# Kernel optimization log

Measured on AMD Instinct MI355X. Metric: run time of the kernel, lower is better.

Reference implementation:

```python
import jax, jax.numpy as jnp
import numpy as np

IMG = 448
GRID = 32          # num_grids = image_size // patch_size
HID = 1024         # mm_hidden_size
B = 64
# (expert_input_image_size, expert_patch, expert_hidden)
EXPERTS = [(448, 14, 1024), (336, 14, 768), (448, 32, 1152)]


def resize_ac(x, oh, ow):
    """Bilinear resize with align_corners=True on last two dims. x: [..., H, W]."""
    h, w = x.shape[-2], x.shape[-1]
    if (h, w) == (oh, ow):
        return x
    ys = jnp.linspace(0.0, h - 1.0, oh)
    xs = jnp.linspace(0.0, w - 1.0, ow)
    y0 = jnp.floor(ys).astype(jnp.int32); y1 = jnp.clip(y0 + 1, 0, h - 1)
    x0 = jnp.floor(xs).astype(jnp.int32); x1 = jnp.clip(x0 + 1, 0, w - 1)
    ty = (ys - y0).astype(x.dtype); tx = (xs - x0).astype(x.dtype)
    rows = x[..., y0, :] * (1 - ty)[:, None] + x[..., y1, :] * ty[:, None]  # [..., oh, W]
    return rows[..., x0] * (1 - tx) + rows[..., x1] * tx                     # [..., oh, ow]


def _forward(x, selected_experts, routing_weights, towers):
    b = x.shape[0]
    out = jnp.zeros((b, GRID * GRID * HID), x.dtype)
    for i, (s, p, c) in enumerate(EXPERTS):
        wt, bt, wp, bp = towers[i]
        xi = resize_ac(x, s, s)  # resize input if expert image size differs (identity otherwise)
        g = s // p
        # patch-embed vision tower: [b,3,s,s] -> [b, g*g, 3*p*p] -> [b, g*g, c]
        patches = xi.reshape(b, 3, g, p, g, p).transpose(0, 2, 4, 1, 3, 5).reshape(b, g * g, 3 * p * p)
        feat = patches @ wt + bt
        # 3D -> [b, c, g, g], resize feature grid to shared num_grids
        feat = feat.transpose(0, 2, 1).reshape(b, c, g, g)
        feat = resize_ac(feat, GRID, GRID)
        # projector over tokens: [b, T, c] @ [c, HID]
        feat = feat.reshape(b, c, GRID * GRID).transpose(0, 2, 1) @ wp + bp
        feat = feat.reshape(b, -1)
        # dense-masked combine (== torch.where gather/scatter with disjoint top-k experts)
        w_i = jnp.sum(jnp.where(selected_experts == i, routing_weights,
                                jnp.zeros((), routing_weights.dtype)), axis=1)
        out = out + w_i[:, None] * feat
    return out.reshape(b, GRID * GRID, HID)


def setup_inputs() -> dict:
    key = jax.random.key(0)
    ks = jax.random.split(key, 20)
    inp = {}
    inp["x"] = jax.random.normal(ks[0], (B, 3, IMG, IMG), jnp.float32)
    # top-2 of 3 experts per sample, distinct within a row (matches scatter semantics)
    e0 = jax.random.randint(ks[1], (B, 1), 0, 3)
    e1 = (e0 + 1 + jax.random.randint(ks[2], (B, 1), 0, 2)) % 3
    inp["selected_experts"] = jnp.concatenate([e0, e1], axis=1)
    rw = jax.random.uniform(ks[3], (B, 2), jnp.float32)
    inp["routing_weights"] = rw / rw.sum(axis=1, keepdims=True)
    for i, (s, p, c) in enumerate(EXPERTS):
        inp[f"w_tower_{i}"] = 0.02 * jax.random.normal(ks[4 + 4 * i], (3 * p * p, c), jnp.float32)
        inp[f"b_tower_{i}"] = jnp.zeros((c,), jnp.float32)
        inp[f"w_proj_{i}"] = 0.02 * jax.random.normal(ks[5 + 4 * i], (c, HID), jnp.float32)
        inp[f"b_proj_{i}"] = jnp.zeros((HID,), jnp.float32)
    return inp


def reference(x, selected_experts, routing_weights,
              w_tower_0, b_tower_0, w_proj_0, b_proj_0,
              w_tower_1, b_tower_1, w_proj_1, b_proj_1,
              w_tower_2, b_tower_2, w_proj_2, b_proj_2):
    towers = [(w_tower_0, b_tower_0, w_proj_0, b_proj_0),
              (w_tower_1, b_tower_1, w_proj_1, b_proj_1),
              (w_tower_2, b_tower_2, w_proj_2, b_proj_2)]
    return _forward(x, selected_experts, routing_weights, towers)
```

## Files before the change

kernel.cpp:

```cpp
#include <hip/hip_runtime.h>
#include <cstddef>
#include <cstdint>


#define HID 1024

typedef __bf16 bf16x8 __attribute__((ext_vector_type(8)));
typedef float f32x4 __attribute__((ext_vector_type(4)));

__device__ __forceinline__ unsigned short f2bf(float f) {
  union { float f; unsigned u; } v; v.f = f;
  unsigned r = v.u + 0x7fffu + ((v.u >> 16) & 1u);
  return (unsigned short)(r >> 16);
}
__device__ __forceinline__ float bf2f(unsigned h) {
  union { unsigned u; float f; } v; v.u = h << 16;
  return v.f;
}
__device__ __forceinline__ void gld16(const unsigned short* g, unsigned short* l) {
  auto gp = (const __attribute__((address_space(1))) unsigned int*)(const void*)g;
  auto lp = (__attribute__((address_space(3))) unsigned int*)(void*)l;
  __builtin_amdgcn_global_load_lds(gp, lp, 16, 0, 0);
}

__device__ __forceinline__ int2 swz128() {
  int gx = gridDim.x;
  int nwg = gx * gridDim.y;
  int lin = (int)(blockIdx.y * gx + blockIdx.x);
  int q = nwg >> 3, r = nwg & 7;
  int xcd = lin & 7, idx = lin >> 3;
  int wg = (xcd < r ? xcd * (q + 1) : r * (q + 1) + (xcd - r) * q) + idx;
  return make_int2((wg % gx) * 128, (wg / gx) * 128);
}

__global__ void k_weights(const int* __restrict__ sel, const float* __restrict__ rw,
                          float* __restrict__ w3) {
  int b = threadIdx.x;
  if (b < 64) {
    float w0 = 0.f, w1 = 0.f, w2 = 0.f;
    for (int k = 0; k < 2; ++k) {
      int e = sel[b * 2 + k];
      float r = rw[b * 2 + k];
      if (e == 0) w0 += r; else if (e == 1) w1 += r; else w2 += r;
    }
    w3[b * 3 + 0] = w0; w3[b * 3 + 1] = w1; w3[b * 3 + 2] = w2;
  }
}

__global__ void k_cbias(const float* __restrict__ w3, const float* __restrict__ b0,
                        const float* __restrict__ b1, const float* __restrict__ b2,
                        float* __restrict__ cb) {
  int s = blockIdx.x;
  float w0 = w3[s * 3], w1 = w3[s * 3 + 1], w2 = w3[s * 3 + 2];
  for (int n = threadIdx.x; n < HID; n += 256)
    cb[s * HID + n] = w0 * b0[n] + w1 * b1[n] + w2 * b2[n];
}

__global__ void k_tables(int* __restrict__ koff, int* __restrict__ rowoff,
                         int4* __restrict__ stok, float4* __restrict__ wco,
                         int S, int P, int G, int T, int bch, int K, int Kp) {
  int idx = blockIdx.x * 256 + threadIdx.x;
  if (idx < Kp) {
    if (idx < K) {
      int pp = P * P;
      int ch = idx / pp;
      int r = idx - ch * pp;
      int py = r / P;
      int px = r - py * P;
      koff[idx] = ch * S * S + py * S + px;
    } else koff[idx] = 0;
  }
  int nro = bch * T;
  if (idx < nro) {
    int bl = idx / T;
    int t = idx - bl * T;
    int gy = t / G;
    int gx = t - gy * G;
    rowoff[idx] = bl * 3 * S * S + gy * P * S + gx * P;
  }
  if (idx < 1024) {
    int oy = idx >> 5, ox = idx & 31;
    float sc = (float)(G - 1) / 31.0f;
    float fy = oy * sc, fx = ox * sc;
    int y0 = (int)floorf(fy), x0 = (int)floorf(fx);
    float ty = fy - y0, tx = fx - x0;
    int y1 = min(y0 + 1, G - 1), x1 = min(x0 + 1, G - 1);
    stok[idx] = make_int4(y0 * G + x0, y0 * G + x1, y1 * G + x0, y1 * G + x1);
    wco[idx] = make_float4((1.f - ty) * (1.f - tx), (1.f - ty) * tx,
                           ty * (1.f - tx), ty * tx);
  }
}

__global__ void k_resize_img(const float* __restrict__ x, unsigned short* __restrict__ o,
                             int total) {
  int idx = blockIdx.x * 256 + threadIdx.x;
  if (idx >= total) return;
  int ox = idx % 336;
  int t = idx / 336;
  int oy = t % 336;
  int bc = t / 336;
  const float sc = 447.0f / 335.0f;
  float fy = oy * sc, fx = ox * sc;
  int y0 = (int)floorf(fy), x0 = (int)floorf(fx);
  float ty = fy - y0, tx = fx - x0;
  int y1 = min(y0 + 1, 447), x1 = min(x0 + 1, 447);
  const float* p = x + (size_t)bc * 448 * 448;
  float v00 = p[y0 * 448 + x0], v01 = p[y0 * 448 + x1];
  float v10 = p[y1 * 448 + x0], v11 = p[y1 * 448 + x1];
  float r0 = v00 * (1.f - ty) + v10 * ty;
  float r1 = v01 * (1.f - ty) + v11 * ty;
  o[idx] = f2bf(r0 * (1.f - tx) + r1 * tx);
}

__global__ void k_pack_w(const float* __restrict__ W, unsigned short* __restrict__ Wp,
                         int K, int N, int Kp) {
  __shared__ float t[32][33];
  int kb = blockIdx.x * 32, nb = blockIdx.y * 32;
  int tx = threadIdx.x & 31, ty = threadIdx.x >> 5;
#pragma unroll
  for (int r = 0; r < 32; r += 8) {
    int k = kb + ty + r, n = nb + tx;
    t[ty + r][tx] = (k < K) ? W[(size_t)k * N + n] : 0.f;
  }
  __syncthreads();
#pragma unroll
  for (int r = 0; r < 32; r += 8) {
    int n = nb + ty + r, k = kb + tx;
    if (k < Kp) Wp[(size_t)n * Kp + k] = f2bf(t[tx][ty + r]);
  }
}

__global__ void k_im2col_f32(const float* __restrict__ img, unsigned short* __restrict__ Ap,
                             const int* __restrict__ rowoff, const int* __restrict__ koff,
                             int M, int K, int Kp) {
  int k2 = (blockIdx.y * 256 + threadIdx.x) * 2;
  if (k2 >= Kp) return;
  int m = blockIdx.x;
  unsigned v = 0;
  if (m < M && k2 < K) {
    float2 f = *(const float2*)(const void*)&img[rowoff[m] + koff[k2]];
    v = (unsigned)f2bf(f.x) | ((unsigned)f2bf(f.y) << 16);
  }
  *(unsigned*)(void*)&Ap[(size_t)m * Kp + k2] = v;
}

__global__ void k_im2col_bf16(const unsigned short* __restrict__ img,
                              unsigned short* __restrict__ Ap,
                              const int* __restrict__ rowoff, const int* __restrict__ koff,
                              int M, int K, int Kp) {
  int k2 = (blockIdx.y * 256 + threadIdx.x) * 2;
  if (k2 >= Kp) return;
  int m = blockIdx.x;
  unsigned v = 0;
  if (m < M && k2 < K)
    v = *(const unsigned*)(const void*)&img[rowoff[m] + koff[k2]];
  *(unsigned*)(void*)&Ap[(size_t)m * Kp + k2] = v;
}

__global__ __launch_bounds__(256) void k_tower(
    const unsigned short* __restrict__ Ap, const unsigned short* __restrict__ Wp,
    const float* __restrict__ bias, unsigned short* __restrict__ Fp,
    int N, int Kp) {
  __shared__ __align__(16) unsigned short As[128 * 32];
  __shared__ __align__(16) unsigned short Bs[128 * 32];
  int tid = threadIdx.x, wave = tid >> 6, lane = tid & 63;
  int2 sw = swz128();
  int n0 = sw.x, m0 = sw.y;

  const unsigned short* arow0 = Ap + (size_t)(m0 + (tid >> 2)) * Kp + (tid & 3) * 8;
  const unsigned short* arow1 = arow0 + (size_t)64 * Kp;
  const unsigned short* wrow0 = Wp + (size_t)(n0 + (tid >> 2)) * Kp + (tid & 3) * 8;
  const unsigned short* wrow1 = wrow0 + (size_t)64 * Kp;
  unsigned short* AsW0 = As + wave * 512;
  unsigned short* AsW1 = As + 2048 + wave * 512;
  unsigned short* BsW0 = Bs + wave * 512;
  unsigned short* BsW1 = Bs + 2048 + wave * 512;

  int wm = (wave >> 1) << 6, wn = (wave & 1) << 6;
  int fm = lane & 15, fq = (lane >> 4) << 3;
  f32x4 acc[4][4] = {};

  for (int kb = 0; kb < Kp; kb += 32) {
    __syncthreads();
    gld16(arow0 + kb, AsW0);
    gld16(arow1 + kb, AsW1);
    gld16(wrow0 + kb, BsW0);
    gld16(wrow1 + kb, BsW1);
    __syncthreads();
    bf16x8 af[4], bfr[4];
#pragma unroll
    for (int i = 0; i < 4; ++i) af[i] = *(const bf16x8*)&As[(wm + i * 16 + fm) * 32 + fq];
#pragma unroll
    for (int j = 0; j < 4; ++j) bfr[j] = *(const bf16x8*)&Bs[(wn + j * 16 + fm) * 32 + fq];
#pragma unroll
    for (int i = 0; i < 4; ++i)
#pragma unroll
      for (int j = 0; j < 4; ++j)
        acc[i][j] = __builtin_amdgcn_mfma_f32_16x16x32_bf16(af[i], bfr[j], acc[i][j], 0, 0, 0);
  }

  int mq = (lane >> 4) << 2;
#pragma unroll
  for (int i = 0; i < 4; ++i) {
    int mbase = m0 + wm + i * 16 + mq;
#pragma unroll
    for (int j = 0; j < 4; ++j) {
      int n = n0 + wn + j * 16 + fm;
      float bsv = bias[n];
      f32x4 v = acc[i][j];
#pragma unroll
      for (int r = 0; r < 4; ++r)
        Fp[(size_t)(mbase + r) * N + n] = f2bf(v[r] + bsv);
    }
  }
}

__global__ void k_feat_resize(const unsigned short* __restrict__ C1,
                              unsigned short* __restrict__ F,
                              const int4* __restrict__ stok, const float4* __restrict__ wco,
                              int Tsrc, int C) {
  int bt = blockIdx.x;
  int bl = bt >> 10, t = bt & 1023;
  int4 s = stok[t];
  float4 w = wco[t];
  const unsigned* b32 = (const unsigned*)(C1 + (size_t)bl * Tsrc * C);
  unsigned* o32 = (unsigned*)(F + (size_t)bt * C);
  int C2 = C >> 1;
  int r0 = s.x * C2, r1 = s.y * C2, r2 = s.z * C2, r3 = s.w * C2;
  for (int c = threadIdx.x; c < C2; c += 256) {
    unsigned p0 = b32[r0 + c], p1 = b32[r1 + c], p2 = b32[r2 + c], p3 = b32[r3 + c];
    float lo = w.x * bf2f(p0 & 0xffffu) + w.y * bf2f(p1 & 0xffffu) +
               w.z * bf2f(p2 & 0xffffu) + w.w * bf2f(p3 & 0xffffu);
    float hi = w.x * bf2f(p0 >> 16) + w.y * bf2f(p1 >> 16) +
               w.z * bf2f(p2 >> 16) + w.w * bf2f(p3 >> 16);
    o32[c] = (unsigned)f2bf(lo) | ((unsigned)f2bf(hi) << 16);
  }
}

__global__ __launch_bounds__(256) void k_proj3(
    const unsigned short* __restrict__ A0, const unsigned short* __restrict__ A1,
    const unsigned short* __restrict__ A2,
    const unsigned short* __restrict__ W0, const unsigned short* __restrict__ W1,
    const unsigned short* __restrict__ W2,
    const float* __restrict__ cb, float* __restrict__ out,
    const float* __restrict__ w3, int b0) {
  __shared__ __align__(16) unsigned short As[128 * 32];
  __shared__ __align__(16) unsigned short Bs[128 * 32];
  int tid = threadIdx.x, wave = tid >> 6, lane = tid & 63;
  int2 sw = swz128();
  int n0 = sw.x, m0 = sw.y;
  int s = b0 + (m0 >> 10);
  float wg0 = w3[s * 3], wg1 = w3[s * 3 + 1], wg2 = w3[s * 3 + 2];
  const float wgs[3] = {wg0, wg1, wg2};
  const unsigned short* Ae[3] = {A0, A1, A2};
  const unsigned short* We[3] = {W0, W1, W2};
  const int Ke[3] = {1024, 768, 1152};

  unsigned short* AsW0 = As + wave * 512;
  unsigned short* AsW1 = As + 2048 + wave * 512;
  unsigned short* BsW0 = Bs + wave * 512;
  unsigned short* BsW1 = Bs + 2048 + wave * 512;
  int wm = (wave >> 1) << 6, wn = (wave & 1) << 6;
  int fm = lane & 15, fq = (lane >> 4) << 3;

  f32x4 accT[4][4] = {};

#pragma unroll
  for (int e = 0; e < 3; ++e) {
    float w = wgs[e];
    if (w == 0.f) continue;
    int K = Ke[e];
    const unsigned short* arow0 = Ae[e] + (size_t)(m0 + (tid >> 2)) * K + (tid & 3) * 8;
    const unsigned short* arow1 = arow0 + (size_t)64 * K;
    const unsigned short* wrow0 = We[e] + (size_t)(n0 + (tid >> 2)) * K + (tid & 3) * 8;
    const unsigned short* wrow1 = wrow0 + (size_t)64 * K;
    f32x4 acc[4][4] = {};
    for (int kb = 0; kb < K; kb += 32) {
      __syncthreads();
      gld16(arow0 + kb, AsW0);
      gld16(arow1 + kb, AsW1);
      gld16(wrow0 + kb, BsW0);
      gld16(wrow1 + kb, BsW1);
      __syncthreads();
      bf16x8 af[4], bfr[4];
#pragma unroll
      for (int i = 0; i < 4; ++i) af[i] = *(const bf16x8*)&As[(wm + i * 16 + fm) * 32 + fq];
#pragma unroll
      for (int j = 0; j < 4; ++j) bfr[j] = *(const bf16x8*)&Bs[(wn + j * 16 + fm) * 32 + fq];
#pragma unroll
      for (int i = 0; i < 4; ++i)
#pragma unroll
        for (int j = 0; j < 4; ++j)
          acc[i][j] = __builtin_amdgcn_mfma_f32_16x16x32_bf16(af[i], bfr[j], acc[i][j], 0, 0, 0);
    }
#pragma unroll
    for (int i = 0; i < 4; ++i)
#pragma unroll
      for (int j = 0; j < 4; ++j)
        accT[i][j] += w * acc[i][j];
  }

  int mq = (lane >> 4) << 2;
  float* obase = out + ((size_t)b0 * 1024 + (size_t)m0) * HID + n0;
  const float* cbs = cb + (size_t)s * HID + n0;
#pragma unroll
  for (int i = 0; i < 4; ++i) {
#pragma unroll
    for (int j = 0; j < 4; ++j) {
      int n = wn + j * 16 + fm;
      float cbv = cbs[n];
      f32x4 v = accT[i][j];
#pragma unroll
      for (int r = 0; r < 4; ++r)
        obase[(size_t)(wm + i * 16 + mq + r) * HID + n] = v[r] + cbv;
    }
  }
}

extern "C" void kernel_launch(void* const* d_in, const int* in_sizes, int n_in,
                              void* d_out, int out_size, void* d_ws, size_t ws_size,
                              hipStream_t stream) {
  (void)in_sizes; (void)n_in; (void)out_size;
  const float* x = (const float*)d_in[0];
  const int* sel = (const int*)d_in[1];
  const float* rw = (const float*)d_in[2];
  const float* wt[3] = {(const float*)d_in[3], (const float*)d_in[7], (const float*)d_in[11]};
  const float* bt[3] = {(const float*)d_in[4], (const float*)d_in[8], (const float*)d_in[12]};
  const float* wp[3] = {(const float*)d_in[5], (const float*)d_in[9], (const float*)d_in[13]};
  const float* bp[3] = {(const float*)d_in[6], (const float*)d_in[10], (const float*)d_in[14]};
  float* out = (float*)d_out;

  char* ws = (char*)d_ws;
  size_t off = 0;
  auto alloc = [&](size_t bytes) -> void* {
    off = (off + 255) & ~(size_t)255;
    void* p = ws + off;
    off += bytes;
    return p;
  };
  auto ceil128 = [](size_t m) -> size_t { return (m + 127) & ~(size_t)127; };

  float* w3 = (float*)alloc(64 * 3 * 4);
  float* cb = (float*)alloc((size_t)64 * HID * 4);
  int* koff0 = (int*)alloc(608 * 4);
  int* koff1 = (int*)alloc(608 * 4);
  int* koff2 = (int*)alloc(3072 * 4);
  int* ro0 = (int*)alloc((size_t)64 * 1024 * 4);
  int* ro1 = (int*)alloc((size_t)64 * 576 * 4);
  int* ro2 = (int*)alloc((size_t)64 * 196 * 4);
  int4* st1 = (int4*)alloc(1024 * 16);
  float4* wc1 = (float4*)alloc(1024 * 16);
  int4* st2 = (int4*)alloc(1024 * 16);
  float4* wc2 = (float4*)alloc(1024 * 16);
  unsigned short* wt0p = (unsigned short*)alloc((size_t)1024 * 608 * 2);
  unsigned short* wt1p = (unsigned short*)alloc((size_t)768 * 608 * 2);
  unsigned short* wt2p = (unsigned short*)alloc((size_t)1152 * 3072 * 2);
  unsigned short* wp0p = (unsigned short*)alloc((size_t)1024 * 1024 * 2);
  unsigned short* wp1p = (unsigned short*)alloc((size_t)1024 * 768 * 2);
  unsigned short* wp2p = (unsigned short*)alloc((size_t)1024 * 1152 * 2);
  size_t fixed_end = off;

  auto scratch_elems = [&](int bc) -> size_t {
    size_t a0 = (size_t)bc * 1024 * 608;
    size_t a1 = (size_t)bc * 3 * 336 * 336 + ceil128((size_t)bc * 576) * 608;
    size_t a2 = ceil128((size_t)bc * 196) * (3072 + 1152);
    size_t m = a0 > a1 ? a0 : a1;
    return m > a2 ? m : a2;
  };
  auto need = [&](int bc) -> size_t {
    size_t el = (size_t)bc * 1024 * (1024 + 768 + 1152) + scratch_elems(bc);
    return el * 2 + 16 * 512;
  };
  int bch = 64;
  while (bch > 1 && fixed_end + need(bch) > ws_size) bch >>= 1;
  unsigned short* F0 = (unsigned short*)alloc((size_t)bch * 1024 * 1024 * 2);
  unsigned short* F1 = (unsigned short*)alloc((size_t)bch * 1024 * 768 * 2);
  unsigned short* F2 = (unsigned short*)alloc((size_t)bch * 1024 * 1152 * 2);
  unsigned short* scratch = (unsigned short*)alloc(scratch_elems(bch) * 2);

  int M1 = bch * 576, Mp1 = (int)ceil128((size_t)M1);
  int M2 = bch * 196, Mp2 = (int)ceil128((size_t)M2);
  unsigned short* x336 = scratch;
  unsigned short* Apad1 = scratch + (size_t)bch * 3 * 336 * 336;
  unsigned short* Apad2 = scratch;
  unsigned short* Ftow2 = scratch + (size_t)Mp2 * 3072;
  unsigned short* Ftow1 = F2;

  k_weights<<<1, 64, 0, stream>>>(sel, rw, w3);
  k_cbias<<<64, 256, 0, stream>>>(w3, bp[0], bp[1], bp[2], cb);
  {
    int n0 = max(608, max(bch * 1024, 1024));
    int n1 = max(608, max(bch * 576, 1024));
    int n2 = max(3072, max(bch * 196, 1024));
    k_tables<<<(n0 + 255) / 256, 256, 0, stream>>>(koff0, ro0, st1, wc1, 448, 14, 32, 1024, bch, 588, 608);
    k_tables<<<(n1 + 255) / 256, 256, 0, stream>>>(koff1, ro1, st1, wc1, 336, 14, 24, 576, bch, 588, 608);
    k_tables<<<(n2 + 255) / 256, 256, 0, stream>>>(koff2, ro2, st2, wc2, 448, 32, 14, 196, bch, 3072, 3072);
  }
  k_pack_w<<<dim3(608 / 32, 1024 / 32), 256, 0, stream>>>(wt[0], wt0p, 588, 1024, 608);
  k_pack_w<<<dim3(608 / 32, 768 / 32), 256, 0, stream>>>(wt[1], wt1p, 588, 768, 608);
  k_pack_w<<<dim3(3072 / 32, 1152 / 32), 256, 0, stream>>>(wt[2], wt2p, 3072, 1152, 3072);
  k_pack_w<<<dim3(1024 / 32, 1024 / 32), 256, 0, stream>>>(wp[0], wp0p, 1024, 1024, 1024);
  k_pack_w<<<dim3(768 / 32, 1024 / 32), 256, 0, stream>>>(wp[1], wp1p, 768, 1024, 768);
  k_pack_w<<<dim3(1152 / 32, 1024 / 32), 256, 0, stream>>>(wp[2], wp2p, 1152, 1024, 1152);

  int nchunk = 64 / bch;
  for (int c = 0; c < nchunk; ++c) {
    int b0 = c * bch;
    const float* xc = x + (size_t)b0 * 3 * 448 * 448;

    {
      int M = bch * 1024;
      k_im2col_f32<<<dim3(M, 2), 256, 0, stream>>>(xc, scratch, ro0, koff0, M, 588, 608);
      k_tower<<<dim3(1024 / 128, M / 128), 256, 0, stream>>>(scratch, wt0p, bt[0], F0, 1024, 608);
    }
    {
      int tot = bch * 3 * 336 * 336;
      k_resize_img<<<(tot + 255) / 256, 256, 0, stream>>>(xc, x336, tot);
      k_im2col_bf16<<<dim3(Mp1, 2), 256, 0, stream>>>(x336, Apad1, ro1, koff1, M1, 588, 608);
      k_tower<<<dim3(768 / 128, Mp1 / 128), 256, 0, stream>>>(Apad1, wt1p, bt[1], Ftow1, 768, 608);
      k_feat_resize<<<bch * 1024, 256, 0, stream>>>(Ftow1, F1, st1, wc1, 576, 768);
    }
    {
      k_im2col_f32<<<dim3(Mp2, 6), 256, 0, stream>>>(xc, Apad2, ro2, koff2, M2, 3072, 3072);
      k_tower<<<dim3(1152 / 128, Mp2 / 128), 256, 0, stream>>>(Apad2, wt2p, bt[2], Ftow2, 1152, 3072);
      k_feat_resize<<<bch * 1024, 256, 0, stream>>>(Ftow2, F2, st2, wc2, 196, 1152);
    }
    k_proj3<<<dim3(HID / 128, bch * 1024 / 128), 256, 0, stream>>>(
        F0, F1, F2, wp0p, wp1p, wp2p, cb, out, w3, b0);
  }
}
```

Baseline: 1.551 ms.

## Project before resizing for experts 1/2 and skip work for unrouted samples

Bilinear feature-grid resize is linear and commutes with the token projection. So experts 1 and 2 now run the projection GEMM on their native 576/196 tokens instead of 1024 resized tokens, and the resize and weighted combine happen on fp32 outputs in a new combine kernel. Image resize, im2col, tower and projection kernels now return early for samples whose routing weight for that expert is zero, which removes unrouted work. This adds an fp32 intermediate buffer and extra read-modify-write traffic on the output. The order of rounding and bias application also changes slightly.

```diff
diff --git a/kernel.cpp b/kernel.cpp
--- a/kernel.cpp
+++ b/kernel.cpp
@@ -92,13 +92,13 @@
 }
 
 __global__ void k_resize_img(const float* __restrict__ x, unsigned short* __restrict__ o,
-                             int total) {
+                             int total, const float* __restrict__ w3, int b0) {
   int idx = blockIdx.x * 256 + threadIdx.x;
   if (idx >= total) return;
+  int bc = idx / (336 * 336);
+  if (w3[(b0 + bc / 3) * 3 + 1] == 0.f) return;
   int ox = idx % 336;
-  int t = idx / 336;
-  int oy = t % 336;
-  int bc = t / 336;
+  int oy = (idx / 336) % 336;
   const float sc = 447.0f / 335.0f;
   float fy = oy * sc, fx = ox * sc;
   int y0 = (int)floorf(fy), x0 = (int)floorf(fx);
@@ -132,12 +132,15 @@
 
 __global__ void k_im2col_f32(const float* __restrict__ img, unsigned short* __restrict__ Ap,
                              const int* __restrict__ rowoff, const int* __restrict__ koff,
-                             int M, int K, int Kp) {
+                             int M, int K, int Kp,
+                             const float* __restrict__ w3, int b0, int e, int T) {
+  int m = blockIdx.x;
+  if (m >= M) return;
+  if (w3[(b0 + m / T) * 3 + e] == 0.f) return;
   int k2 = (blockIdx.y * 256 + threadIdx.x) * 2;
   if (k2 >= Kp) return;
-  int m = blockIdx.x;
   unsigned v = 0;
-  if (m < M && k2 < K) {
+  if (k2 < K) {
     float2 f = *(const float2*)(const void*)&img[rowoff[m] + koff[k2]];
     v = (unsigned)f2bf(f.x) | ((unsigned)f2bf(f.y) << 16);
   }
@@ -147,12 +150,15 @@
 __global__ void k_im2col_bf16(const unsigned short* __restrict__ img,
                               unsigned short* __restrict__ Ap,
                               const int* __restrict__ rowoff, const int* __restrict__ koff,
-                              int M, int K, int Kp) {
+                              int M, int K, int Kp,
+                              const float* __restrict__ w3, int b0, int e, int T) {
+  int m = blockIdx.x;
+  if (m >= M) return;
+  if (w3[(b0 + m / T) * 3 + e] == 0.f) return;
   int k2 = (blockIdx.y * 256 + threadIdx.x) * 2;
   if (k2 >= Kp) return;
-  int m = blockIdx.x;
   unsigned v = 0;
-  if (m < M && k2 < K)
+  if (k2 < K)
     v = *(const unsigned*)(const void*)&img[rowoff[m] + koff[k2]];
   *(unsigned*)(void*)&Ap[(size_t)m * Kp + k2] = v;
 }
@@ -160,12 +166,20 @@
 __global__ __launch_bounds__(256) void k_tower(
     const unsigned short* __restrict__ Ap, const unsigned short* __restrict__ Wp,
     const float* __restrict__ bias, unsigned short* __restrict__ Fp,
-    int N, int Kp) {
+    int N, int Kp, const float* __restrict__ w3, int b0, int e, int T, int bch) {
   __shared__ __align__(16) unsigned short As[128 * 32];
   __shared__ __align__(16) unsigned short Bs[128 * 32];
   int tid = threadIdx.x, wave = tid >> 6, lane = tid & 63;
   int2 sw = swz128();
   int n0 = sw.x, m0 = sw.y;
+
+  {
+    int s0 = m0 / T, s1 = (m0 + 127) / T;
+    if (s1 >= bch) s1 = bch - 1;
+    bool act = false;
+    for (int s = s0; s <= s1; ++s) act |= (w3[(b0 + s) * 3 + e] != 0.f);
+    if (!act) return;
+  }
 
   const unsigned short* arow0 = Ap + (size_t)(m0 + (tid >> 2)) * Kp + (tid & 3) * 8;
   const unsigned short* arow1 = arow0 + (size_t)64 * Kp;
@@ -215,33 +229,8 @@
   }
 }
 
-__global__ void k_feat_resize(const unsigned short* __restrict__ C1,
-                              unsigned short* __restrict__ F,
-                              const int4* __restrict__ stok, const float4* __restrict__ wco,
-                              int Tsrc, int C) {
-  int bt = blockIdx.x;
-  int bl = bt >> 10, t = bt & 1023;
-  int4 s = stok[t];
-  float4 w = wco[t];
-  const unsigned* b32 = (const unsigned*)(C1 + (size_t)bl * Tsrc * C);
-  unsigned* o32 = (unsigned*)(F + (size_t)bt * C);
-  int C2 = C >> 1;
-  int r0 = s.x * C2, r1 = s.y * C2, r2 = s.z * C2, r3 = s.w * C2;
-  for (int c = threadIdx.x; c < C2; c += 256) {
-    unsigned p0 = b32[r0 + c], p1 = b32[r1 + c], p2 = b32[r2 + c], p3 = b32[r3 + c];
-    float lo = w.x * bf2f(p0 & 0xffffu) + w.y * bf2f(p1 & 0xffffu) +
-               w.z * bf2f(p2 & 0xffffu) + w.w * bf2f(p3 & 0xffffu);
-    float hi = w.x * bf2f(p0 >> 16) + w.y * bf2f(p1 >> 16) +
-               w.z * bf2f(p2 >> 16) + w.w * bf2f(p3 >> 16);
-    o32[c] = (unsigned)f2bf(lo) | ((unsigned)f2bf(hi) << 16);
-  }
-}
-
-__global__ __launch_bounds__(256) void k_proj3(
-    const unsigned short* __restrict__ A0, const unsigned short* __restrict__ A1,
-    const unsigned short* __restrict__ A2,
-    const unsigned short* __restrict__ W0, const unsigned short* __restrict__ W1,
-    const unsigned short* __restrict__ W2,
+__global__ __launch_bounds__(256) void k_proj0(
+    const unsigned short* __restrict__ A, const unsigned short* __restrict__ W,
     const float* __restrict__ cb, float* __restrict__ out,
     const float* __restrict__ w3, int b0) {
   __shared__ __align__(16) unsigned short As[128 * 32];
@@ -250,71 +239,159 @@
   int2 sw = swz128();
   int n0 = sw.x, m0 = sw.y;
   int s = b0 + (m0 >> 10);
-  float wg0 = w3[s * 3], wg1 = w3[s * 3 + 1], wg2 = w3[s * 3 + 2];
-  const float wgs[3] = {wg0, wg1, wg2};
-  const unsigned short* Ae[3] = {A0, A1, A2};
-  const unsigned short* We[3] = {W0, W1, W2};
-  const int Ke[3] = {1024, 768, 1152};
-
+  float w0 = w3[s * 3];
+  float* obase = out + ((size_t)b0 * 1024 + (size_t)m0) * HID + n0;
+  const float* cbs = cb + (size_t)s * HID + n0;
+  if (w0 == 0.f) {
+    for (int idx = tid; idx < 128 * 32; idx += 256) {
+      int rr = idx >> 5, cc = (idx & 31) << 2;
+      *(float4*)&obase[(size_t)rr * HID + cc] = *(const float4*)&cbs[cc];
+    }
+    return;
+  }
+  const int K = 1024;
+  const unsigned short* arow0 = A + (size_t)(m0 + (tid >> 2)) * K + (tid & 3) * 8;
+  const unsigned short* arow1 = arow0 + (size_t)64 * K;
+  const unsigned short* wrow0 = W + (size_t)(n0 + (tid >> 2)) * K + (tid & 3) * 8;
+  const unsigned short* wrow1 = wrow0 + (size_t)64 * K;
   unsigned short* AsW0 = As + wave * 512;
   unsigned short* AsW1 = As + 2048 + wave * 512;
   unsigned short* BsW0 = Bs + wave * 512;
   unsigned short* BsW1 = Bs + 2048 + wave * 512;
   int wm = (wave >> 1) << 6, wn = (wave & 1) << 6;
   int fm = lane & 15, fq = (lane >> 4) << 3;
-
-  f32x4 accT[4][4] = {};
-
-#pragma unroll
-  for (int e = 0; e < 3; ++e) {
-    float w = wgs[e];
-    if (w == 0.f) continue;
-    int K = Ke[e];
-    const unsigned short* arow0 = Ae[e] + (size_t)(m0 + (tid >> 2)) * K + (tid & 3) * 8;
-    const unsigned short* arow1 = arow0 + (size_t)64 * K;
-    const unsigned short* wrow0 = We[e] + (size_t)(n0 + (tid >> 2)) * K + (tid & 3) * 8;
-    const unsigned short* wrow1 = wrow0 + (size_t)64 * K;
-    f32x4 acc[4][4] = {};
-    for (int kb = 0; kb < K; kb += 32) {
-      __syncthreads();
-      gld16(arow0 + kb, AsW0);
-      gld16(arow1 + kb, AsW1);
-      gld16(wrow0 + kb, BsW0);
-      gld16(wrow1 + kb, BsW1);
-      __syncthreads();
-      bf16x8 af[4], bfr[4];
-#pragma unroll
-      for (int i = 0; i < 4; ++i) af[i] = *(const bf16x8*)&As[(wm + i * 16 + fm) * 32 + fq];
-#pragma unroll
-      for (int j = 0; j < 4; ++j) bfr[j] = *(const bf16x8*)&Bs[(wn + j * 16 + fm) * 32 + fq];
-#pragma unroll
-      for (int i = 0; i < 4; ++i)
-#pragma unroll
-        for (int j = 0; j < 4; ++j)
-          acc[i][j] = __builtin_amdgcn_mfma_f32_16x16x32_bf16(af[i], bfr[j], acc[i][j], 0, 0, 0);
-    }
+  f32x4 acc[4][4] = {};
+  for (int kb = 0; kb < K; kb += 32) {
+    __syncthreads();
+    gld16(arow0 + kb, AsW0);
+    gld16(arow1 + kb, AsW1);
+    gld16(wrow0 + kb, BsW0);
+    gld16(wrow1 + kb, BsW1);
+    __syncthreads();
+    bf16x8 af[4], bfr[4];
+#pragma unroll
+    for (int i = 0; i < 4; ++i) af[i] = *(const bf16x8*)&As[(wm + i * 16 + fm) * 32 + fq];
+#pragma unroll
+    for (int j = 0; j < 4; ++j) bfr[j] = *(const bf16x8*)&Bs[(wn + j * 16 + fm) * 32 + fq];
 #pragma unroll
     for (int i = 0; i < 4; ++i)
 #pragma unroll
       for (int j = 0; j < 4; ++j)
-        accT[i][j] += w * acc[i][j];
-  }
-
+        acc[i][j] = __builtin_amdgcn_mfma_f32_16x16x32_bf16(af[i], bfr[j], acc[i][j], 0, 0, 0);
+  }
   int mq = (lane >> 4) << 2;
-  float* obase = out + ((size_t)b0 * 1024 + (size_t)m0) * HID + n0;
-  const float* cbs = cb + (size_t)s * HID + n0;
 #pragma unroll
   for (int i = 0; i < 4; ++i) {
 #pragma unroll
     for (int j = 0; j < 4; ++j) {
       int n = wn + j * 16 + fm;
       float cbv = cbs[n];
-      f32x4 v = accT[i][j];
+      f32x4 v = acc[i][j];
 #pragma unroll
       for (int r = 0; r < 4; ++r)
-        obase[(size_t)(wm + i * 16 + mq + r) * HID + n] = v[r] + cbv;
-    }
-  }
+        obase[(size_t)(wm + i * 16 + mq + r) * HID + n] = w0 * v[r] + cbv;
+    }
+  }
+}
+
+__global__ __launch_bounds__(256) void k_projP(
+    const unsigned short* __restrict__ A, const unsigned short* __restrict__ W,
+    float* __restrict__ P, const float* __restrict__ w3,
+    int b0, int e, int T, int bch, int K) {
+  __shared__ __align__(16) unsigned short As[128 * 32];
+  __shared__ __align__(16) unsigned short Bs[128 * 32];
+  int tid = threadIdx.x, wave = tid >> 6, lane = tid & 63;
+  int2 sw = swz128();
+  int n0 = sw.x, m0 = sw.y;
+  {
+    int s0 = m0 / T, s1 = (m0 + 127) / T;
+    if (s1 >= bch) s1 = bch - 1;
+    bool act = false;
+    for (int s = s0; s <= s1; ++s) act |= (w3[(b0 + s) * 3 + e] != 0.f);
+    if (!act) return;
+  }
+  const unsigned short* arow0 = A + (size_t)(m0 + (tid >> 2)) * K + (tid & 3) * 8;
+  const unsigned short* arow1 = arow0 + (size_t)64 * K;
+  const unsigned short* wrow0 = W + (size_t)(n0 + (tid >> 2)) * K + (tid & 3) * 8;
+  const unsigned short* wrow1 = wrow0 + (size_t)64 * K;
+  unsigned short* AsW0 = As + wave * 512;
+  unsigned short* AsW1 = As + 2048 + wave * 512;
+  unsigned short* BsW0 = Bs + wave * 512;
+  unsigned short* BsW1 = Bs + 2048 + wave * 512;
+  int wm = (wave >> 1) << 6, wn = (wave & 1) << 6;
+  int fm = lane & 15, fq = (lane >> 4) << 3;
+  f32x4 acc[4][4] = {};
+  for (int kb = 0; kb < K; kb += 32) {
+    __syncthreads();
+    gld16(arow0 + kb, AsW0);
+    gld16(arow1 + kb, AsW1);
+    gld16(wrow0 + kb, BsW0);
+    gld16(wrow1 + kb, BsW1);
+    __syncthreads();
+    bf16x8 af[4], bfr[4];
+#pragma unroll
+    for (int i = 0; i < 4; ++i) af[i] = *(const bf16x8*)&As[(wm + i * 16 + fm) * 32 + fq];
+#pragma unroll
+    for (int j = 0; j < 4; ++j) bfr[j] = *(const bf16x8*)&Bs[(wn + j * 16 + fm) * 32 + fq];
+#pragma unroll
+    for (int i = 0; i < 4; ++i)
+#pragma unroll
+      for (int j = 0; j < 4; ++j)
+        acc[i][j] = __builtin_amdgcn_mfma_f32_16x16x32_bf16(af[i], bfr[j], acc[i][j], 0, 0, 0);
+  }
+  int mq = (lane >> 4) << 2;
+#pragma unroll
+  for (int i = 0; i < 4; ++i) {
+#pragma unroll
+    for (int j = 0; j < 4; ++j) {
+      int n = n0 + wn + j * 16 + fm;
+      f32x4 v = acc[i][j];
+#pragma unroll
+      for (int r = 0; r < 4; ++r)
+        P[(size_t)(m0 + wm + i * 16 + mq + r) * HID + n] = v[r];
+    }
+  }
+}
+
+__global__ void k_combine(float* __restrict__ out,
+                          const float* __restrict__ P1, const float* __restrict__ P2,
+                          const int4* __restrict__ st1, const float4* __restrict__ wc1,
+                          const int4* __restrict__ st2, const float4* __restrict__ wc2,
+                          const float* __restrict__ w3, int b0) {
+  int nwg = gridDim.x;
+  int lin = blockIdx.x;
+  int q = nwg >> 3;
+  int bt = (lin & 7) * q + (lin >> 3);
+  int s = bt >> 10, t = bt & 1023;
+  float w1 = w3[(b0 + s) * 3 + 1], w2 = w3[(b0 + s) * 3 + 2];
+  int n = threadIdx.x << 2;
+  float* op = out + ((size_t)(b0 + s) * 1024 + t) * HID + n;
+  float4 acc = *(float4*)op;
+  if (w1 != 0.f) {
+    int4 si = st1[t]; float4 wc = wc1[t];
+    const float* base = P1 + (size_t)s * 576 * HID + n;
+    float4 a = *(const float4*)&base[(size_t)si.x * HID];
+    float4 b = *(const float4*)&base[(size_t)si.y * HID];
+    float4 c = *(const float4*)&base[(size_t)si.z * HID];
+    float4 d = *(const float4*)&base[(size_t)si.w * HID];
+    acc.x += w1 * (wc.x * a.x + wc.y * b.x + wc.z * c.x + wc.w * d.x);
+    acc.y += w1 * (wc.x * a.y + wc.y * b.y + wc.z * c.y + wc.w * d.y);
+    acc.z += w1 * (wc.x * a.z + wc.y * b.z + wc.z * c.z + wc.w * d.z);
+    acc.w += w1 * (wc.x * a.w + wc.y * b.w + wc.z * c.w + wc.w * d.w);
+  }
+  if (w2 != 0.f) {
+    int4 si = st2[t]; float4 wc = wc2[t];
+    const float* base = P2 + (size_t)s * 196 * HID + n;
+    float4 a = *(const float4*)&base[(size_t)si.x * HID];
+    float4 b = *(const float4*)&base[(size_t)si.y * HID];
+    float4 c = *(const float4*)&base[(size_t)si.z * HID];
+    float4 d = *(const float4*)&base[(size_t)si.w * HID];
+    acc.x += w2 * (wc.x * a.x + wc.y * b.x + wc.z * c.x + wc.w * d.x);
+    acc.y += w2 * (wc.x * a.y + wc.y * b.y + wc.z * c.y + wc.w * d.y);
+    acc.z += w2 * (wc.x * a.z + wc.y * b.z + wc.z * c.z + wc.w * d.z);
+    acc.w += w2 * (wc.x * a.w + wc.y * b.w + wc.z * c.w + wc.w * d.w);
+  }
+  *(float4*)op = acc;
 }
 
 extern "C" void kernel_launch(void* const* d_in, const int* in_sizes, int n_in,
@@ -361,30 +438,32 @@
   size_t fixed_end = off;
 
   auto scratch_elems = [&](int bc) -> size_t {
-    size_t a0 = (size_t)bc * 1024 * 608;
-    size_t a1 = (size_t)bc * 3 * 336 * 336 + ceil128((size_t)bc * 576) * 608;
-    size_t a2 = ceil128((size_t)bc * 196) * (3072 + 1152);
-    size_t m = a0 > a1 ? a0 : a1;
-    return m > a2 ? m : a2;
+    size_t mp1 = ceil128((size_t)bc * 576), mp2 = ceil128((size_t)bc * 196);
+    size_t p0 = (size_t)bc * 1024 * 1024 + (size_t)bc * 1024 * 608;
+    size_t p1 = (size_t)bc * 338688 + mp1 * 608 + mp1 * 768;
+    size_t p2 = mp2 * 3072 + mp2 * 1152;
+    size_t m = p0 > p1 ? p0 : p1;
+    return m > p2 ? m : p2;
   };
   auto need = [&](int bc) -> size_t {
-    size_t el = (size_t)bc * 1024 * (1024 + 768 + 1152) + scratch_elems(bc);
-    return el * 2 + 16 * 512;
+    size_t mp1 = ceil128((size_t)bc * 576), mp2 = ceil128((size_t)bc * 196);
+    return scratch_elems(bc) * 2 + (mp1 + mp2) * (size_t)HID * 4 + 32 * 512;
   };
   int bch = 64;
   while (bch > 1 && fixed_end + need(bch) > ws_size) bch >>= 1;
-  unsigned short* F0 = (unsigned short*)alloc((size_t)bch * 1024 * 1024 * 2);
-  unsigned short* F1 = (unsigned short*)alloc((size_t)bch * 1024 * 768 * 2);
-  unsigned short* F2 = (unsigned short*)alloc((size_t)bch * 1024 * 1152 * 2);
+
+  size_t Mp1 = ceil128((size_t)bch * 576), Mp2 = ceil128((size_t)bch * 196);
   unsigned short* scratch = (unsigned short*)alloc(scratch_elems(bch) * 2);
-
-  int M1 = bch * 576, Mp1 = (int)ceil128((size_t)M1);
-  int M2 = bch * 196, Mp2 = (int)ceil128((size_t)M2);
+  float* P1 = (float*)alloc(Mp1 * HID * 4);
+  float* P2 = (float*)alloc(Mp2 * HID * 4);
+
+  unsigned short* Ftow0 = scratch;
+  unsigned short* Apad0 = scratch + (size_t)bch * 1024 * 1024;
   unsigned short* x336 = scratch;
-  unsigned short* Apad1 = scratch + (size_t)bch * 3 * 336 * 336;
+  unsigned short* Apad1 = scratch + (size_t)bch * 338688;
+  unsigned short* Ftow1 = Apad1 + Mp1 * 608;
   unsigned short* Apad2 = scratch;
-  unsigned short* Ftow2 = scratch + (size_t)Mp2 * 3072;
-  unsigned short* Ftow1 = F2;
+  unsigned short* Ftow2 = scratch + Mp2 * 3072;
 
   k_weights<<<1, 64, 0, stream>>>(sel, rw, w3);
   k_cbias<<<64, 256, 0, stream>>>(w3, bp[0], bp[1], bp[2], cb);
@@ -410,22 +489,32 @@
 
     {
       int M = bch * 1024;
-      k_im2col_f32<<<dim3(M, 2), 256, 0, stream>>>(xc, scratch, ro0, koff0, M, 588, 608);
-      k_tower<<<dim3(1024 / 128, M / 128), 256, 0, stream>>>(scratch, wt0p, bt[0], F0, 1024, 608);
+      k_im2col_f32<<<dim3(M, 2), 256, 0, stream>>>(xc, Apad0, ro0, koff0, M, 588, 608,
+                                                   w3, b0, 0, 1024);
+      k_tower<<<dim3(1024 / 128, M / 128), 256, 0, stream>>>(Apad0, wt0p, bt[0], Ftow0,
+                                                             1024, 608, w3, b0, 0, 1024, bch);
+      k_proj0<<<dim3(HID / 128, M / 128), 256, 0, stream>>>(Ftow0, wp0p, cb, out, w3, b0);
     }
     {
       int tot = bch * 3 * 336 * 336;
-      k_resize_img<<<(tot + 255) / 256, 256, 0, stream>>>(xc, x336, tot);
-      k_im2col_bf16<<<dim3(Mp1, 2), 256, 0, stream>>>(x336, Apad1, ro1, koff1, M1, 588, 608);
-      k_tower<<<dim3(768 / 128, Mp1 / 128), 256, 0, stream>>>(Apad1, wt1p, bt[1], Ftow1, 768, 608);
-      k_feat_resize<<<bch * 1024, 256, 0, stream>>>(Ftow1, F1, st1, wc1, 576, 768);
+      int M = bch * 576;
+      k_resize_img<<<(tot + 255) / 256, 256, 0, stream>>>(xc, x336, tot, w3, b0);
+      k_im2col_bf16<<<dim3(M, 2), 256, 0, stream>>>(x336, Apad1, ro1, koff1, M, 588, 608,
+                                                    w3, b0, 1, 576);
+      k_tower<<<dim3(768 / 128, (int)(Mp1 / 128)), 256, 0, stream>>>(
+          Apad1, wt1p, bt[1], Ftow1, 768, 608, w3, b0, 1, 576, bch);
+      k_projP<<<dim3(HID / 128, (int)(Mp1 / 128)), 256, 0, stream>>>(
+          Ftow1, wp1p, P1, w3, b0, 1, 576, bch, 768);
     }
     {
-      k_im2col_f32<<<dim3(Mp2, 6), 256, 0, stream>>>(xc, Apad2, ro2, koff2, M2, 3072, 3072);
-      k_tower<<<dim3(1152 / 128, Mp2 / 128), 256, 0, stream>>>(Apad2, wt2p, bt[2], Ftow2, 1152, 3072);
-      k_feat_resize<<<bch * 1024, 256, 0, stream>>>(Ftow2, F2, st2, wc2, 196, 1152);
-    }
-    k_proj3<<<dim3(HID / 128, bch * 1024 / 128), 256, 0, stream>>>(
-        F0, F1, F2, wp0p, wp1p, wp2p, cb, out, w3, b0);
-  }
-}
+      int M = bch * 196;
+      k_im2col_f32<<<dim3(M, 6), 256, 0, stream>>>(xc, Apad2, ro2, koff2, M, 3072, 3072,
+                                                   w3, b0, 2, 196);
+      k_tower<<<dim3(1152 / 128, (int)(Mp2 / 128)), 256, 0, stream>>>(
+          Apad2, wt2p, bt[2], Ftow2, 1152, 3072, w3, b0, 2, 196, bch);
+      k_projP<<<dim3(HID / 128, (int)(Mp2 / 128)), 256, 0, stream>>>(
+          Ftow2, wp2p, P2, w3, b0, 2, 196, bch, 1152);
+    }
+    k_combine<<<bch * 1024, 256, 0, stream>>>(out, P1, P2, st1, wc1, st2, wc2, w3, b0);
+  }
+}
```

New measurement: 1.370 ms. -11.7%, faster.
